# Kernel tuning notes

Hardware: AMD Instinct MI355X
Metric: run time of the kernel (lower is better)

Reference implementation:

```python
import jax, jax.numpy as jnp
import numpy as np
from jax import lax

B, C, HT, HC, S = 4, 128, 256, 256, 4   # tissue batch, channels, tissue HW, cell HW, scale_factor
ORIGIN = 1024                            # hard-coded self.origin_shape


def setup_inputs() -> dict:
    key = jax.random.key(0)
    k1, k2, k3, k4, k5 = jax.random.split(key, 5)
    tissue_features = jax.random.normal(k1, (B, C, HT, HT), jnp.float32)
    cell_features = jax.random.normal(k2, (1, C, HC, HC), jnp.float32)
    # loc in [128, 896] so the ROI (half-width 32 at tissue res 256) stays in-bounds
    loc = jax.random.randint(k3, (B, 2), 128, 897, dtype=jnp.int32)
    conv_w = jax.random.normal(k4, (C, C, 3, 3), jnp.float32) * 0.02
    conv_b = jax.random.normal(k5, (C,), jnp.float32) * 0.02
    return {"tissue_features": tissue_features, "cell_features": cell_features,
            "loc": loc, "conv_w": conv_w, "conv_b": conv_b}


def _forward(tissue, cell, conv_w, conv_b, loc):
    Bb, Cc, H, W = tissue.shape
    # conv3x3, padding=1 (SAME)
    origin = lax.conv_general_dilated(
        cell, conv_w, window_strides=(1, 1), padding='SAME',
        dimension_numbers=('NCHW', 'OIHW', 'NCHW')) + conv_b[None, :, None, None]
    # AvgPool2d(kernel=stride=S) via reshape-mean; cell batch is 1
    hp, wp = origin.shape[2] // S, origin.shape[3] // S
    avg = origin.reshape(1, Cc, hp, S, wp, S).mean(axis=(3, 5))[0]  # [C, hp, wp] == [C, 2l, 2l]
    l = (128 * W) // ORIGIN                      # half ROI width (static)
    tx = (loc[:, 1] * W) // ORIGIN               # note: x = loc[:,1], y = loc[:,0]
    ty = (loc[:, 0] * W) // ORIGIN

    def upd(tf_j, txj, tyj):
        start = (0, txj - l, tyj - l)
        roi = lax.dynamic_slice(tf_j, start, (Cc, 2 * l, 2 * l))
        return lax.dynamic_update_slice(tf_j, roi + avg, start)

    final = jax.vmap(upd)(tissue, tx, ty)        # each sample's ROI gets avg added once
    # the torch loop appends the same (fully mutated) tensor B times then stacks
    return jnp.broadcast_to(final[None], (Bb,) + final.shape)


def reference(tissue_features, cell_features, loc, conv_w, conv_b):
    return _forward(tissue_features, cell_features, conv_w, conv_b, loc)
```

## Files before the change

kernel.cpp:

```cpp
#include <hip/hip_runtime.h>

typedef float nf4 __attribute__((ext_vector_type(4)));


#define CLS 258
#define CSS 260

__global__ __launch_bounds__(256) void k_prep(const float* __restrict__ w,
                                              float* __restrict__ wT2,
                                              const float* __restrict__ cell,
                                              float* __restrict__ box) {
    if (blockIdx.x < 576) {
        int idx = blockIdx.x * 256 + threadIdx.x;
        int c  = idx & 127;
        int k  = (idx >> 7) % 9;
        int ci = idx / (9 * 128);
        wT2[idx] = w[(c * 128 + ci) * 9 + k];
        return;
    }
    __shared__ float cl[35 * CLS];
    __shared__ float cs[24 * CSS];
    int sid = blockIdx.x - 576;
    int ci = sid >> 3;
    int s  = sid & 7;
    int tid = threadIdx.x;
    int r0 = 32 * s - 1;
    const float* base = cell + (size_t)ci * 65536;

#pragma unroll
    for (int r = 0; r < 35; ++r) {
        int gr = r0 + r;
        float val = (gr >= 0 && gr < 256) ? base[gr * 256 + tid] : 0.f;
        cl[r * CLS + 1 + tid] = val;
    }
    if (tid < 35) { cl[tid * CLS] = 0.f; cl[tid * CLS + 257] = 0.f; }
    __syncthreads();

    for (int q = tid; q < 24 * 258; q += 256) {
        int r24 = q / 258, c = q % 258;
        int yyl = (r24 / 3) * 4 + (r24 % 3);
        int lr = yyl;
        cs[r24 * CSS + c] = cl[lr * CLS + c] + cl[(lr + 1) * CLS + c] +
                            cl[(lr + 2) * CLS + c] + cl[(lr + 3) * CLS + c];
    }
    __syncthreads();

#pragma unroll
    for (int k = 0; k < 6; ++k) {
        int o = tid + 256 * k;
        int xt = o & 63;
        int r24 = o >> 6;
        int yyl = (r24 / 3) * 4 + (r24 % 3);
        nf4 v0 = *(const nf4*)&cs[r24 * CSS + 4 * xt];
        nf4 v1 = *(const nf4*)&cs[r24 * CSS + 4 * xt + 4];
        float4 ov;
        ov.x = v0[0] + v0[1] + v0[2] + v0[3];
        ov.y = v0[1] + v0[2] + v0[3] + v1[0];
        ov.z = v0[2] + v0[3] + v1[0] + v1[1];
        ov.w = v0[3] + v1[0] + v1[1] + v1[2];
        *(float4*)(box + (size_t)ci * 65536 + (32 * s + yyl) * 256 + 4 * xt) = ov;
    }
}

__global__ __launch_bounds__(256) void k_gemm(const float* __restrict__ box,
                                              const float* __restrict__ wT2,
                                              float* __restrict__ part) {
    __shared__ float wlds[2][1152];
    __shared__ float boxlds[2][768];
    int i     = blockIdx.x;
    int split = blockIdx.y;
    int tid = threadIdx.x;
    int cg  = tid & 31;
    int pg  = tid >> 5;

    float acc[4][8];
#pragma unroll
    for (int a = 0; a < 4; ++a)
#pragma unroll
        for (int p = 0; p < 8; ++p) acc[a][p] = 0.f;

    int ci0 = split * 16;

    auto stage = [&](int ci, int buf) {
        const float* bsrc = box + (size_t)ci * 65536 + (4 * i) * 256;
#pragma unroll
        for (int s = 0; s < 3; ++s)
            boxlds[buf][tid + 256 * s] = bsrc[tid + 256 * s];
        const float* wsrc = wT2 + (size_t)ci * 1152;
#pragma unroll
        for (int s = 0; s < 5; ++s) {
            int q = tid + 256 * s;
            if (q < 1152) wlds[buf][q] = wsrc[q];
        }
    };

    stage(ci0, 0);
    for (int t = 0; t < 16; ++t) {
        __syncthreads();
        if (t < 15) stage(ci0 + t + 1, (t + 1) & 1);
        int b = t & 1;

        nf4 wv[9];
#pragma unroll
        for (int k = 0; k < 9; ++k)
            wv[k] = *(const nf4*)&wlds[b][k * 128 + 4 * cg];

#pragma unroll
        for (int p = 0; p < 8; ++p) {
            int j = 8 * pg + p;
            nf4 b0 = *(const nf4*)&boxlds[b][0 * 256 + 4 * j];
            nf4 b1 = *(const nf4*)&boxlds[b][1 * 256 + 4 * j];
            nf4 b2 = *(const nf4*)&boxlds[b][2 * 256 + 4 * j];
#pragma unroll
            for (int a = 0; a < 4; ++a) {
                float sm = acc[a][p];
                sm = fmaf(wv[0][a], b0[0], sm);
                sm = fmaf(wv[1][a], b0[1], sm);
                sm = fmaf(wv[2][a], b0[2], sm);
                sm = fmaf(wv[3][a], b1[0], sm);
                sm = fmaf(wv[4][a], b1[1], sm);
                sm = fmaf(wv[5][a], b1[2], sm);
                sm = fmaf(wv[6][a], b2[0], sm);
                sm = fmaf(wv[7][a], b2[1], sm);
                sm = fmaf(wv[8][a], b2[2], sm);
                acc[a][p] = sm;
            }
        }
    }

    float* dst = part + (size_t)split * (128 * 4096);
#pragma unroll
    for (int a = 0; a < 4; ++a) {
        int c = 4 * cg + a;
        float* row = dst + (size_t)c * 4096 + i * 64 + 8 * pg;
        float4 lo = make_float4(acc[a][0], acc[a][1], acc[a][2], acc[a][3]);
        float4 hi = make_float4(acc[a][4], acc[a][5], acc[a][6], acc[a][7]);
        *(float4*)(row)     = lo;
        *(float4*)(row + 4) = hi;
    }
}

__global__ __launch_bounds__(256) void k_avgfin(const float* __restrict__ part,
                                                const float* __restrict__ bias,
                                                float* __restrict__ avg) {
    int idx4 = blockIdx.x * 256 + threadIdx.x;
    int c = idx4 >> 10;
    nf4 s = {0.f, 0.f, 0.f, 0.f};
#pragma unroll
    for (int sp = 0; sp < 8; ++sp) {
        nf4 v = *(const nf4*)(part + (size_t)sp * 524288 + (size_t)idx4 * 4);
        s += v;
    }
    float b = bias[c];
    nf4 o = s * 0.0625f + b;
    *(nf4*)(avg + (size_t)idx4 * 4) = o;
}

__global__ __launch_bounds__(256) void k_out(const float* __restrict__ tissue,
                                             const float* __restrict__ avg,
                                             const int* __restrict__ loc,
                                             float* __restrict__ out) {
    int idx4 = blockIdx.x * 256 + threadIdx.x;
    size_t f = (size_t)idx4 * 4;
    int j   = idx4 >> 21;
    int r4  = idx4 & ((1 << 21) - 1);
    int c   = r4 >> 14;
    int hw4 = r4 & 16383;
    int h   = hw4 >> 6;
    int w0  = (hw4 & 63) << 2;

    nf4 v = __builtin_nontemporal_load((const nf4*)(tissue + f));

    int sh = (loc[2 * j + 1] >> 2) - 32;
    int sw = (loc[2 * j]     >> 2) - 32;
    int ah = h - sh;
    if (ah >= 0 && ah < 64) {
        const float* ar = avg + c * 4096 + ah * 64;
        int aw = w0 - sw;
        if (aw     >= 0 && aw     < 64) v[0] += ar[aw];
        if (aw + 1 >= 0 && aw + 1 < 64) v[1] += ar[aw + 1];
        if (aw + 2 >= 0 && aw + 2 < 64) v[2] += ar[aw + 2];
        if (aw + 3 >= 0 && aw + 3 < 64) v[3] += ar[aw + 3];
    }
#pragma unroll
    for (int b = 0; b < 4; ++b)
        __builtin_nontemporal_store(v, (nf4*)(out + (size_t)b * 33554432 + f));
}

extern "C" void kernel_launch(void* const* d_in, const int* in_sizes, int n_in,
                              void* d_out, int out_size, void* d_ws, size_t ws_size,
                              hipStream_t stream) {
    const float* tissue = (const float*)d_in[0];
    const float* cell   = (const float*)d_in[1];
    const int*   loc    = (const int*)d_in[2];
    const float* w      = (const float*)d_in[3];
    const float* bias   = (const float*)d_in[4];
    float* out = (float*)d_out;

    char* wsb = (char*)d_ws;
    float* box  = (float*)(wsb);
    float* wT2  = (float*)(wsb + 33554432);
    float* part = (float*)(wsb + 34144256);
    float* avg  = (float*)(wsb + 50921472);

    k_prep<<<1600, 256, 0, stream>>>(w, wT2, cell, box);
    k_gemm<<<dim3(64, 8), 256, 0, stream>>>(box, wT2, part);
    k_avgfin<<<512, 256, 0, stream>>>(part, bias, avg);
    k_out<<<32768, 256, 0, stream>>>(tissue, avg, loc, out);
}
```

Measured before the change: 181.2 us.

## Fuse box-sum prep into conv GEMM and double the channel split

Removes the separate prep kernel that precomputed the 4x4 box-summed cell tensor and transposed weights. The GEMM kernel now loads six raw cell rows per input channel, forms the vertical and horizontal box sums in shared memory, and gathers weights directly. The input-channel split goes from 8 to 16 so more blocks run the GEMM, and the final reduction sums 16 partials. This drops a 32 MB intermediate write and read and one launch, at the cost of losing double-buffered staging, adding extra barriers, strided weight gathers, and more partial-sum traffic.

```diff
diff --git a/kernel.cpp b/kernel.cpp
--- a/kernel.cpp
+++ b/kernel.cpp
@@ -3,75 +3,25 @@
 typedef float nf4 __attribute__((ext_vector_type(4)));
 
 
-#define CLS 258
-#define CSS 260
+#define NSPLIT 16
+#define CIPS   8
 
-__global__ __launch_bounds__(256) void k_prep(const float* __restrict__ w,
-                                              float* __restrict__ wT2,
-                                              const float* __restrict__ cell,
-                                              float* __restrict__ box) {
-    if (blockIdx.x < 576) {
-        int idx = blockIdx.x * 256 + threadIdx.x;
-        int c  = idx & 127;
-        int k  = (idx >> 7) % 9;
-        int ci = idx / (9 * 128);
-        wT2[idx] = w[(c * 128 + ci) * 9 + k];
-        return;
-    }
-    __shared__ float cl[35 * CLS];
-    __shared__ float cs[24 * CSS];
-    int sid = blockIdx.x - 576;
-    int ci = sid >> 3;
-    int s  = sid & 7;
-    int tid = threadIdx.x;
-    int r0 = 32 * s - 1;
-    const float* base = cell + (size_t)ci * 65536;
-
-#pragma unroll
-    for (int r = 0; r < 35; ++r) {
-        int gr = r0 + r;
-        float val = (gr >= 0 && gr < 256) ? base[gr * 256 + tid] : 0.f;
-        cl[r * CLS + 1 + tid] = val;
-    }
-    if (tid < 35) { cl[tid * CLS] = 0.f; cl[tid * CLS + 257] = 0.f; }
-    __syncthreads();
-
-    for (int q = tid; q < 24 * 258; q += 256) {
-        int r24 = q / 258, c = q % 258;
-        int yyl = (r24 / 3) * 4 + (r24 % 3);
-        int lr = yyl;
-        cs[r24 * CSS + c] = cl[lr * CLS + c] + cl[(lr + 1) * CLS + c] +
-                            cl[(lr + 2) * CLS + c] + cl[(lr + 3) * CLS + c];
-    }
-    __syncthreads();
-
-#pragma unroll
-    for (int k = 0; k < 6; ++k) {
-        int o = tid + 256 * k;
-        int xt = o & 63;
-        int r24 = o >> 6;
-        int yyl = (r24 / 3) * 4 + (r24 % 3);
-        nf4 v0 = *(const nf4*)&cs[r24 * CSS + 4 * xt];
-        nf4 v1 = *(const nf4*)&cs[r24 * CSS + 4 * xt + 4];
-        float4 ov;
-        ov.x = v0[0] + v0[1] + v0[2] + v0[3];
-        ov.y = v0[1] + v0[2] + v0[3] + v1[0];
-        ov.z = v0[2] + v0[3] + v1[0] + v1[1];
-        ov.w = v0[3] + v1[0] + v1[1] + v1[2];
-        *(float4*)(box + (size_t)ci * 65536 + (32 * s + yyl) * 256 + 4 * xt) = ov;
-    }
-}
-
-__global__ __launch_bounds__(256) void k_gemm(const float* __restrict__ box,
-                                              const float* __restrict__ wT2,
+__global__ __launch_bounds__(256) void k_gemm(const float* __restrict__ cell,
+                                              const float* __restrict__ w,
                                               float* __restrict__ part) {
-    __shared__ float wlds[2][1152];
-    __shared__ float boxlds[2][768];
+    __shared__ float vs[3][260];
+    __shared__ float bx[3][256];
+    __shared__ float wl[1152];
     int i     = blockIdx.x;
     int split = blockIdx.y;
     int tid = threadIdx.x;
     int cg  = tid & 31;
     int pg  = tid >> 5;
+
+    if (tid < 9) {
+        int dy = tid / 3, q = tid % 3;
+        vs[dy][q == 0 ? 0 : 256 + q] = 0.f;
+    }
 
     float acc[4][8];
 #pragma unroll
@@ -79,38 +29,41 @@
 #pragma unroll
         for (int p = 0; p < 8; ++p) acc[a][p] = 0.f;
 
-    int ci0 = split * 16;
-
-    auto stage = [&](int ci, int buf) {
-        const float* bsrc = box + (size_t)ci * 65536 + (4 * i) * 256;
+    int r0 = 4 * i - 1;
+    for (int t = 0; t < CIPS; ++t) {
+        int ci = split * CIPS + t;
+        const float* base = cell + (size_t)ci * 65536;
+        float cr[6];
 #pragma unroll
-        for (int s = 0; s < 3; ++s)
-            boxlds[buf][tid + 256 * s] = bsrc[tid + 256 * s];
-        const float* wsrc = wT2 + (size_t)ci * 1152;
+        for (int r = 0; r < 6; ++r) {
+            int row = r0 + r;
+            cr[r] = ((unsigned)row < 256u) ? base[row * 256 + tid] : 0.f;
+        }
+        __syncthreads();
+        vs[0][tid + 1] = cr[0] + cr[1] + cr[2] + cr[3];
+        vs[1][tid + 1] = cr[1] + cr[2] + cr[3] + cr[4];
+        vs[2][tid + 1] = cr[2] + cr[3] + cr[4] + cr[5];
 #pragma unroll
         for (int s = 0; s < 5; ++s) {
             int q = tid + 256 * s;
-            if (q < 1152) wlds[buf][q] = wsrc[q];
+            if (q < 1152)
+                wl[q] = w[(size_t)(q & 127) * 1152 + (size_t)ci * 9 + (q >> 7)];
         }
-    };
-
-    stage(ci0, 0);
-    for (int t = 0; t < 16; ++t) {
         __syncthreads();
-        if (t < 15) stage(ci0 + t + 1, (t + 1) & 1);
-        int b = t & 1;
-
+#pragma unroll
+        for (int dy = 0; dy < 3; ++dy)
+            bx[dy][tid] = vs[dy][tid] + vs[dy][tid + 1] + vs[dy][tid + 2] + vs[dy][tid + 3];
+        __syncthreads();
         nf4 wv[9];
 #pragma unroll
         for (int k = 0; k < 9; ++k)
-            wv[k] = *(const nf4*)&wlds[b][k * 128 + 4 * cg];
-
+            wv[k] = *(const nf4*)&wl[k * 128 + 4 * cg];
 #pragma unroll
         for (int p = 0; p < 8; ++p) {
             int j = 8 * pg + p;
-            nf4 b0 = *(const nf4*)&boxlds[b][0 * 256 + 4 * j];
-            nf4 b1 = *(const nf4*)&boxlds[b][1 * 256 + 4 * j];
-            nf4 b2 = *(const nf4*)&boxlds[b][2 * 256 + 4 * j];
+            nf4 b0 = *(const nf4*)&bx[0][4 * j];
+            nf4 b1 = *(const nf4*)&bx[1][4 * j];
+            nf4 b2 = *(const nf4*)&bx[2][4 * j];
 #pragma unroll
             for (int a = 0; a < 4; ++a) {
                 float sm = acc[a][p];
@@ -128,7 +81,7 @@
         }
     }
 
-    float* dst = part + (size_t)split * (128 * 4096);
+    float* dst = part + (size_t)split * 524288;
 #pragma unroll
     for (int a = 0; a < 4; ++a) {
         int c = 4 * cg + a;
@@ -147,12 +100,9 @@
     int c = idx4 >> 10;
     nf4 s = {0.f, 0.f, 0.f, 0.f};
 #pragma unroll
-    for (int sp = 0; sp < 8; ++sp) {
-        nf4 v = *(const nf4*)(part + (size_t)sp * 524288 + (size_t)idx4 * 4);
-        s += v;
-    }
-    float b = bias[c];
-    nf4 o = s * 0.0625f + b;
+    for (int sp = 0; sp < NSPLIT; ++sp)
+        s += *(const nf4*)(part + (size_t)sp * 524288 + (size_t)idx4 * 4);
+    nf4 o = s * 0.0625f + bias[c];
     *(nf4*)(avg + (size_t)idx4 * 4) = o;
 }
 
@@ -160,21 +110,19 @@
                                              const float* __restrict__ avg,
                                              const int* __restrict__ loc,
                                              float* __restrict__ out) {
-    int idx4 = blockIdx.x * 256 + threadIdx.x;
-    size_t f = (size_t)idx4 * 4;
-    int j   = idx4 >> 21;
-    int r4  = idx4 & ((1 << 21) - 1);
-    int c   = r4 >> 14;
-    int hw4 = r4 & 16383;
-    int h   = hw4 >> 6;
-    int w0  = (hw4 & 63) << 2;
+    int bid = blockIdx.x, tid = threadIdx.x;
+    int j = bid >> 13;
+    int c = (bid >> 6) & 127;
+    int h = ((bid << 2) | (tid >> 6)) & 255;
+    int w0 = (tid & 63) << 2;
+    size_t f = ((size_t)bid << 10) | (unsigned)(tid << 2);
 
     nf4 v = __builtin_nontemporal_load((const nf4*)(tissue + f));
 
     int sh = (loc[2 * j + 1] >> 2) - 32;
     int sw = (loc[2 * j]     >> 2) - 32;
     int ah = h - sh;
-    if (ah >= 0 && ah < 64) {
+    if ((unsigned)ah < 64u) {
         const float* ar = avg + c * 4096 + ah * 64;
         int aw = w0 - sw;
         if (aw     >= 0 && aw     < 64) v[0] += ar[aw];
@@ -198,13 +146,10 @@
     float* out = (float*)d_out;
 
     char* wsb = (char*)d_ws;
-    float* box  = (float*)(wsb);
-    float* wT2  = (float*)(wsb + 33554432);
-    float* part = (float*)(wsb + 34144256);
-    float* avg  = (float*)(wsb + 50921472);
+    float* part = (float*)(wsb);
+    float* avg  = (float*)(wsb + 33554432);
 
-    k_prep<<<1600, 256, 0, stream>>>(w, wT2, cell, box);
-    k_gemm<<<dim3(64, 8), 256, 0, stream>>>(box, wT2, part);
+    k_gemm<<<dim3(64, NSPLIT), 256, 0, stream>>>(cell, w, part);
     k_avgfin<<<512, 256, 0, stream>>>(part, bias, avg);
     k_out<<<32768, 256, 0, stream>>>(tissue, avg, loc, out);
 }
```

Result: no change. 182.0 us (+0.5%).
